# Kernel tuning notes

Measured on AMD Instinct MI355X. Metric: run time of the kernel, lower is better.

Reference implementation:

```python
import jax, jax.numpy as jnp
import numpy as np

D = 32        # number of TT cores (d)
R = 16        # tt_rank
B = 262144    # batch size


def setup_inputs() -> dict:
    key = jax.random.key(0)
    k1, k2, k3, k4 = jax.random.split(key, 4)
    return {
        "X": jax.random.randint(k1, (B, D), 0, 2, dtype=jnp.int32),
        "core_first": jax.random.normal(k2, (1, R, 2), dtype=jnp.float32),
        "cores_mid": jax.random.normal(k3, (D - 2, R, R, 2), dtype=jnp.float32),
        "core_last": jax.random.normal(k4, (R, 1, 2), dtype=jnp.float32),
    }


def reference(X, core_first, cores_mid, core_last):
    # First core: cores[0][:, :, X[:,0]] -> [1, R, B] -> permute -> [B, 1, R].
    # We carry the squeezed [B, R] row vector instead of [B, 1, R].
    carry0 = jnp.take(core_first[0], X[:, 0], axis=-1).T  # [B, R]

    def step(carry, inp):
        core, idx = inp                       # core: [R, R, 2], idx: [B]
        c = jnp.take(core, idx, axis=2)       # gathered core: [R, R, B]
        new = jnp.einsum('br,rsb->bs', carry, c)  # batched (1xR)@(RxR)
        return new, None

    # Middle cores i = 1 .. D-2 (sequential chain, data-dependent).
    carry, _ = jax.lax.scan(step, carry0, (cores_mid, X[:, 1:D - 1].T))

    # Last core: cores[-1][:, :, X[:,-1]] -> [R, 1, B]; contract to scalar per batch.
    c_last = jnp.take(core_last[:, 0, :], X[:, -1], axis=-1)  # [R, B]
    out = jnp.einsum('br,rb->b', carry, c_last)               # [B]  (squeeze of [B,1,1])
    return out
```

## Files before the change

kernel.cpp:

```cpp
#include <hip/hip_runtime.h>


#define R 16
#define TT_D 32
#define BATCH 262144

#define OFF_V16  0
#define OFF_W16  1048576
#define OFF_P8   2097152
#define OFF_Q8   (OFF_P8 + 65536)
#define OFF_V8   (OFF_Q8 + 65536)
#define OFF_W8   (OFF_V8 + 4096)
#define OFF_PK   (OFF_W8 + 4096)
#define WS_FLOATS (OFF_PK + BATCH)

#define NBLK1 1024
#define NTAB  34

__device__ __forceinline__ void rowvec_mat(const float* __restrict__ M,
                                           float* __restrict__ u) {
    float nv[R];
    #pragma unroll
    for (int s = 0; s < R; s++) nv[s] = 0.f;
    #pragma unroll
    for (int t2 = 0; t2 < R; t2++) {
        const float a = u[t2];
        #pragma unroll
        for (int s = 0; s < R; s++) nv[s] += a * M[t2 * 16 + s];
    }
    #pragma unroll
    for (int s = 0; s < R; s++) u[s] = nv[s];
}

__device__ __forceinline__ void mat_colvec(const float* __restrict__ M,
                                           float* __restrict__ w) {
    float nw[R];
    #pragma unroll
    for (int r2 = 0; r2 < R; r2++) {
        float a = 0.f;
        #pragma unroll
        for (int k = 0; k < R; k++) a += M[r2 * 16 + k] * w[k];
        nw[r2] = a;
    }
    #pragma unroll
    for (int r2 = 0; r2 < R; r2++) w[r2] = nw[r2];
}

__global__ __launch_bounds__(256) void tt_stage1(const int* __restrict__ X,
                                                 const float* __restrict__ cf,
                                                 const float* __restrict__ cm,
                                                 const float* __restrict__ cl,
                                                 float* __restrict__ ws) {
    __shared__ float scm[8 * 512];
    const int blk = blockIdx.x;
    const int t = threadIdx.x;

    if (blk < NTAB) {
        int cbase, ncore;
        if (blk < 16)       { cbase = 7;  ncore = 8; }
        else if (blk < 32)  { cbase = 15; ncore = 8; }
        else if (blk == 32) { cbase = 0;  ncore = 7; }
        else                { cbase = 23; ncore = 7; }
        const float2* cm2 = (const float2*)(cm + cbase * 512);
        for (int j = t; j < ncore * 256; j += 256) {
            const float2 vv = cm2[j];
            const int ci = j >> 8, idx = j & 255;
            scm[ci * 512 + idx] = vv.x;
            scm[ci * 512 + 256 + idx] = vv.y;
        }
        __syncthreads();

        if (blk < 32) {
            const bool isP = (blk < 16);
            const int e = (isP ? blk : blk - 16) * 16 + (t >> 4), r = t & 15;
            float u[R];
            const float* M0 = scm + ((e >> 7) & 1) * 256;
            #pragma unroll
            for (int s = 0; s < R; s++) u[s] = M0[r * 16 + s];
            for (int k = 1; k < 8; k++)
                rowvec_mat(scm + k * 512 + ((e >> (7 - k)) & 1) * 256, u);
            float* o = ws + (isP ? OFF_P8 : OFF_Q8) + e * 256 + r * 16;
            #pragma unroll
            for (int s = 0; s < R; s++) o[s] = u[s];
        } else if (blk == 32) {
            const int e = t;
            float u[R];
            #pragma unroll
            for (int s = 0; s < R; s++) u[s] = cf[s * 2 + ((e >> 7) & 1)];
            for (int k = 0; k < 7; k++)
                rowvec_mat(scm + k * 512 + ((e >> (6 - k)) & 1) * 256, u);
            float* o = ws + OFF_V8 + e * 16;
            #pragma unroll
            for (int s = 0; s < R; s++) o[s] = u[s];
        } else {
            const int e = t;
            float w[R];
            #pragma unroll
            for (int r2 = 0; r2 < R; r2++) w[r2] = cl[r2 * 2 + (e & 1)];
            for (int j = 6; j >= 0; j--)
                mat_colvec(scm + j * 512 + ((e >> (7 - j)) & 1) * 256, w);
            float* o = ws + OFF_W8 + e * 16;
            #pragma unroll
            for (int r2 = 0; r2 < R; r2++) o[r2] = w[r2];
        }
    } else {
        unsigned* pk = (unsigned*)(ws + OFF_PK);
        const int stride = (NBLK1 - NTAB) * 256;
        for (int b = (blk - NTAB) * 256 + t; b < BATCH; b += stride) {
            const int4* Xr = (const int4*)(X + (size_t)b * TT_D);
            unsigned p = 0, s = 0;
            #pragma unroll
            for (int q = 0; q < 4; q++) {
                const int4 c = Xr[q];
                p = (p << 4) | ((unsigned)(c.x & 1) << 3) | ((unsigned)(c.y & 1) << 2)
                             | ((unsigned)(c.z & 1) << 1) | (unsigned)(c.w & 1);
            }
            #pragma unroll
            for (int q = 4; q < 8; q++) {
                const int4 c = Xr[q];
                s = (s << 4) | ((unsigned)(c.x & 1) << 3) | ((unsigned)(c.y & 1) << 2)
                             | ((unsigned)(c.z & 1) << 1) | (unsigned)(c.w & 1);
            }
            pk[b] = (p << 16) | s;
        }
    }
}

__global__ __launch_bounds__(256) void tt_stage2(float* __restrict__ ws) {
    __shared__ float sQ[256];
    const int blk = blockIdx.x;
    const int t = threadIdx.x;
    if (blk < 256) {
        const int hi = blk, lo = t;
        float u[R];
        const float* v8 = ws + OFF_V8 + hi * 16;
        #pragma unroll
        for (int k = 0; k < R; k++) u[k] = v8[k];
        rowvec_mat(ws + OFF_P8 + lo * 256, u);
        float* o = ws + OFF_V16 + (size_t)(hi * 256 + lo) * 16;
        #pragma unroll
        for (int s = 0; s < R; s++) o[s] = u[s];
    } else {
        const int hi = blk - 256, lo = t;
        sQ[t] = ws[OFF_Q8 + hi * 256 + t];
        __syncthreads();
        float w[R];
        const float* w8 = ws + OFF_W8 + lo * 16;
        #pragma unroll
        for (int k = 0; k < R; k++) w[k] = w8[k];
        mat_colvec(sQ, w);
        float* o = ws + OFF_W16 + (size_t)(hi * 256 + lo) * 16;
        #pragma unroll
        for (int r2 = 0; r2 < R; r2++) o[r2] = w[r2];
    }
}

__global__ __launch_bounds__(256) void tt_gather(const float* __restrict__ ws,
                                                 float* __restrict__ out) {
    const int b = blockIdx.x * 256 + threadIdx.x;
    const unsigned pk = ((const unsigned*)(ws + OFF_PK))[b];
    const unsigned p = pk >> 16, s = pk & 0xffffu;
    const float4* v = (const float4*)(ws + OFF_V16 + (size_t)p * 16);
    const float4* w = (const float4*)(ws + OFF_W16 + (size_t)s * 16);
    float acc = 0.f;
    #pragma unroll
    for (int k = 0; k < 4; k++) {
        const float4 a = v[k], c = w[k];
        acc += a.x * c.x + a.y * c.y + a.z * c.z + a.w * c.w;
    }
    out[b] = acc;
}

__global__ __launch_bounds__(256) void tt_direct(const int* __restrict__ X,
                                                 const float* __restrict__ cf,
                                                 const float* __restrict__ cm,
                                                 const float* __restrict__ cl,
                                                 float* __restrict__ out) {
    __shared__ float scm[30 * 16 * 16 * 2];
    for (int i = threadIdx.x; i < 30 * 16 * 16 * 2; i += blockDim.x) scm[i] = cm[i];
    __syncthreads();
    const int b = blockIdx.x * blockDim.x + threadIdx.x;
    if (b >= BATCH) return;
    const int* xr = X + (size_t)b * TT_D;
    float v[R], nv[R];
    const int x0 = xr[0] & 1;
    #pragma unroll
    for (int rr = 0; rr < R; rr++) v[rr] = cf[rr * 2 + x0];
    for (int i = 1; i <= 30; i++) {
        const int bit = xr[i] & 1;
        const float* M = scm + (i - 1) * 512;
        #pragma unroll
        for (int s2 = 0; s2 < R; s2++) {
            float acc = 0.f;
            #pragma unroll
            for (int rr = 0; rr < R; rr++) acc += v[rr] * M[(rr * 16 + s2) * 2 + bit];
            nv[s2] = acc;
        }
        #pragma unroll
        for (int s2 = 0; s2 < R; s2++) v[s2] = nv[s2];
    }
    const int xl = xr[31] & 1;
    float acc = 0.f;
    #pragma unroll
    for (int rr = 0; rr < R; rr++) acc += v[rr] * cl[rr * 2 + xl];
    out[b] = acc;
}

extern "C" void kernel_launch(void* const* d_in, const int* in_sizes, int n_in,
                              void* d_out, int out_size, void* d_ws, size_t ws_size,
                              hipStream_t stream) {
    const int* X = (const int*)d_in[0];
    const float* cf = (const float*)d_in[1];
    const float* cm = (const float*)d_in[2];
    const float* cl = (const float*)d_in[3];
    float* out = (float*)d_out;

    if (ws_size >= (size_t)WS_FLOATS * sizeof(float)) {
        float* ws = (float*)d_ws;
        tt_stage1<<<NBLK1, 256, 0, stream>>>(X, cf, cm, cl, ws);
        tt_stage2<<<512, 256, 0, stream>>>(ws);
        tt_gather<<<BATCH / 256, 256, 0, stream>>>(ws, out);
    } else {
        tt_direct<<<(BATCH + 255) / 256, 256, 0, stream>>>(X, cf, cm, cl, out);
    }
}
```

Baseline: 117.4 us.

## Fuse three stages into one cooperative kernel with grid syncs

Replaces the three launches (table build with X packing, table expansion, gather) with one cooperative kernel of 512 blocks that uses grid.sync between phases. Each thread packs its two batch elements' bits into registers before the first sync, so the packed-index array no longer goes through global memory. This is meant to remove launch gaps and the pack-array round trip. In exchange it adds two grid-wide barriers, and only 34 blocks do the table work in phase one. The old three-kernel path stays as a fallback if the cooperative launch fails.

Result: slower. 346.0 us (+194.7%).

```diff
diff --git a/kernel.cpp b/kernel.cpp
--- a/kernel.cpp
+++ b/kernel.cpp
@@ -1,21 +1,22 @@
 #include <hip/hip_runtime.h>
+#include <hip/hip_cooperative_groups.h>
+
+namespace cg = cooperative_groups;
 
 
 #define R 16
 #define TT_D 32
 #define BATCH 262144
-
-#define OFF_V16  0
-#define OFF_W16  1048576
-#define OFF_P8   2097152
-#define OFF_Q8   (OFF_P8 + 65536)
+#define NBLK 512
+#define EPB (BATCH / NBLK)
+
+#define OFF_P8   0
+#define OFF_Q8   65536
 #define OFF_V8   (OFF_Q8 + 65536)
 #define OFF_W8   (OFF_V8 + 4096)
-#define OFF_PK   (OFF_W8 + 4096)
-#define WS_FLOATS (OFF_PK + BATCH)
-
-#define NBLK1 1024
-#define NTAB  34
+#define OFF_V16  (OFF_W8 + 4096)
+#define OFF_W16  (OFF_V16 + 1048576)
+#define WS_FLOATS (OFF_W16 + 1048576)
 
 __device__ __forceinline__ void rowvec_mat(const float* __restrict__ M,
                                            float* __restrict__ u) {
@@ -46,16 +47,33 @@
     for (int r2 = 0; r2 < R; r2++) w[r2] = nw[r2];
 }
 
-__global__ __launch_bounds__(256) void tt_stage1(const int* __restrict__ X,
-                                                 const float* __restrict__ cf,
-                                                 const float* __restrict__ cm,
-                                                 const float* __restrict__ cl,
-                                                 float* __restrict__ ws) {
+__device__ __forceinline__ unsigned pack_elem(const int* __restrict__ X, int b) {
+    const int4* Xr = (const int4*)(X + (size_t)b * TT_D);
+    unsigned v = 0;
+    #pragma unroll
+    for (int q = 0; q < 8; q++) {
+        const int4 c = Xr[q];
+        v = (v << 4) | ((unsigned)(c.x & 1) << 3) | ((unsigned)(c.y & 1) << 2)
+                     | ((unsigned)(c.z & 1) << 1) | (unsigned)(c.w & 1);
+    }
+    return v;
+}
+
+__global__ __launch_bounds__(256, 2) void tt_fused(const int* __restrict__ X,
+                                                   const float* __restrict__ cf,
+                                                   const float* __restrict__ cm,
+                                                   const float* __restrict__ cl,
+                                                   float* __restrict__ ws,
+                                                   float* __restrict__ out) {
     __shared__ float scm[8 * 512];
     const int blk = blockIdx.x;
     const int t = threadIdx.x;
-
-    if (blk < NTAB) {
+    cg::grid_group grid = cg::this_grid();
+
+    const unsigned pk0 = pack_elem(X, blk * EPB + t);
+    const unsigned pk1 = pack_elem(X, blk * EPB + 256 + t);
+
+    if (blk < 34) {
         int cbase, ncore;
         if (blk < 16)       { cbase = 7;  ncore = 8; }
         else if (blk < 32)  { cbase = 15; ncore = 8; }
@@ -103,26 +121,122 @@
             #pragma unroll
             for (int r2 = 0; r2 < R; r2++) o[r2] = w[r2];
         }
+    }
+
+    __threadfence();
+    grid.sync();
+
+    if (blk < 256) {
+        float u[R];
+        const float* v8 = ws + OFF_V8 + blk * 16;
+        #pragma unroll
+        for (int k = 0; k < R; k++) u[k] = v8[k];
+        rowvec_mat(ws + OFF_P8 + t * 256, u);
+        float* o = ws + OFF_V16 + (size_t)(blk * 256 + t) * 16;
+        #pragma unroll
+        for (int s = 0; s < R; s++) o[s] = u[s];
     } else {
-        unsigned* pk = (unsigned*)(ws + OFF_PK);
-        const int stride = (NBLK1 - NTAB) * 256;
-        for (int b = (blk - NTAB) * 256 + t; b < BATCH; b += stride) {
-            const int4* Xr = (const int4*)(X + (size_t)b * TT_D);
-            unsigned p = 0, s = 0;
-            #pragma unroll
-            for (int q = 0; q < 4; q++) {
-                const int4 c = Xr[q];
-                p = (p << 4) | ((unsigned)(c.x & 1) << 3) | ((unsigned)(c.y & 1) << 2)
-                             | ((unsigned)(c.z & 1) << 1) | (unsigned)(c.w & 1);
-            }
-            #pragma unroll
-            for (int q = 4; q < 8; q++) {
-                const int4 c = Xr[q];
-                s = (s << 4) | ((unsigned)(c.x & 1) << 3) | ((unsigned)(c.y & 1) << 2)
-                             | ((unsigned)(c.z & 1) << 1) | (unsigned)(c.w & 1);
-            }
-            pk[b] = (p << 16) | s;
-        }
+        const int hi = blk - 256;
+        __syncthreads();
+        scm[t] = ws[OFF_Q8 + hi * 256 + t];
+        __syncthreads();
+        float w[R];
+        const float* w8 = ws + OFF_W8 + t * 16;
+        #pragma unroll
+        for (int k = 0; k < R; k++) w[k] = w8[k];
+        mat_colvec(scm, w);
+        float* o = ws + OFF_W16 + (size_t)(hi * 256 + t) * 16;
+        #pragma unroll
+        for (int r2 = 0; r2 < R; r2++) o[r2] = w[r2];
+    }
+
+    __threadfence();
+    grid.sync();
+
+    {
+        const float4* v = (const float4*)(ws + OFF_V16 + (size_t)(pk0 >> 16) * 16);
+        const float4* w = (const float4*)(ws + OFF_W16 + (size_t)(pk0 & 0xffffu) * 16);
+        float acc = 0.f;
+        #pragma unroll
+        for (int k = 0; k < 4; k++) {
+            const float4 a = v[k], c = w[k];
+            acc += a.x * c.x + a.y * c.y + a.z * c.z + a.w * c.w;
+        }
+        out[blk * EPB + t] = acc;
+    }
+    {
+        const float4* v = (const float4*)(ws + OFF_V16 + (size_t)(pk1 >> 16) * 16);
+        const float4* w = (const float4*)(ws + OFF_W16 + (size_t)(pk1 & 0xffffu) * 16);
+        float acc = 0.f;
+        #pragma unroll
+        for (int k = 0; k < 4; k++) {
+            const float4 a = v[k], c = w[k];
+            acc += a.x * c.x + a.y * c.y + a.z * c.z + a.w * c.w;
+        }
+        out[blk * EPB + 256 + t] = acc;
+    }
+}
+
+__global__ __launch_bounds__(256) void tt_stage1(const int* __restrict__ X,
+                                                 const float* __restrict__ cf,
+                                                 const float* __restrict__ cm,
+                                                 const float* __restrict__ cl,
+                                                 float* __restrict__ ws,
+                                                 unsigned* __restrict__ pk) {
+    __shared__ float scm[8 * 512];
+    const int blk = blockIdx.x;
+    const int t = threadIdx.x;
+    if (blk < 34) {
+        int cbase, ncore;
+        if (blk < 16)       { cbase = 7;  ncore = 8; }
+        else if (blk < 32)  { cbase = 15; ncore = 8; }
+        else if (blk == 32) { cbase = 0;  ncore = 7; }
+        else                { cbase = 23; ncore = 7; }
+        const float2* cm2 = (const float2*)(cm + cbase * 512);
+        for (int j = t; j < ncore * 256; j += 256) {
+            const float2 vv = cm2[j];
+            const int ci = j >> 8, idx = j & 255;
+            scm[ci * 512 + idx] = vv.x;
+            scm[ci * 512 + 256 + idx] = vv.y;
+        }
+        __syncthreads();
+        if (blk < 32) {
+            const bool isP = (blk < 16);
+            const int e = (isP ? blk : blk - 16) * 16 + (t >> 4), r = t & 15;
+            float u[R];
+            const float* M0 = scm + ((e >> 7) & 1) * 256;
+            #pragma unroll
+            for (int s = 0; s < R; s++) u[s] = M0[r * 16 + s];
+            for (int k = 1; k < 8; k++)
+                rowvec_mat(scm + k * 512 + ((e >> (7 - k)) & 1) * 256, u);
+            float* o = ws + (isP ? OFF_P8 : OFF_Q8) + e * 256 + r * 16;
+            #pragma unroll
+            for (int s = 0; s < R; s++) o[s] = u[s];
+        } else if (blk == 32) {
+            const int e = t;
+            float u[R];
+            #pragma unroll
+            for (int s = 0; s < R; s++) u[s] = cf[s * 2 + ((e >> 7) & 1)];
+            for (int k = 0; k < 7; k++)
+                rowvec_mat(scm + k * 512 + ((e >> (6 - k)) & 1) * 256, u);
+            float* o = ws + OFF_V8 + e * 16;
+            #pragma unroll
+            for (int s = 0; s < R; s++) o[s] = u[s];
+        } else {
+            const int e = t;
+            float w[R];
+            #pragma unroll
+            for (int r2 = 0; r2 < R; r2++) w[r2] = cl[r2 * 2 + (e & 1)];
+            for (int j = 6; j >= 0; j--)
+                mat_colvec(scm + j * 512 + ((e >> (7 - j)) & 1) * 256, w);
+            float* o = ws + OFF_W8 + e * 16;
+            #pragma unroll
+            for (int r2 = 0; r2 < R; r2++) o[r2] = w[r2];
+        }
+    } else {
+        const int stride = (1024 - 34) * 256;
+        for (int b = (blk - 34) * 256 + t; b < BATCH; b += stride)
+            pk[b] = pack_elem(X, b);
     }
 }
 
@@ -131,37 +245,36 @@
     const int blk = blockIdx.x;
     const int t = threadIdx.x;
     if (blk < 256) {
-        const int hi = blk, lo = t;
         float u[R];
-        const float* v8 = ws + OFF_V8 + hi * 16;
+        const float* v8 = ws + OFF_V8 + blk * 16;
         #pragma unroll
         for (int k = 0; k < R; k++) u[k] = v8[k];
-        rowvec_mat(ws + OFF_P8 + lo * 256, u);
-        float* o = ws + OFF_V16 + (size_t)(hi * 256 + lo) * 16;
+        rowvec_mat(ws + OFF_P8 + t * 256, u);
+        float* o = ws + OFF_V16 + (size_t)(blk * 256 + t) * 16;
         #pragma unroll
         for (int s = 0; s < R; s++) o[s] = u[s];
     } else {
-        const int hi = blk - 256, lo = t;
+        const int hi = blk - 256;
         sQ[t] = ws[OFF_Q8 + hi * 256 + t];
         __syncthreads();
         float w[R];
-        const float* w8 = ws + OFF_W8 + lo * 16;
+        const float* w8 = ws + OFF_W8 + t * 16;
         #pragma unroll
         for (int k = 0; k < R; k++) w[k] = w8[k];
         mat_colvec(sQ, w);
-        float* o = ws + OFF_W16 + (size_t)(hi * 256 + lo) * 16;
+        float* o = ws + OFF_W16 + (size_t)(hi * 256 + t) * 16;
         #pragma unroll
         for (int r2 = 0; r2 < R; r2++) o[r2] = w[r2];
     }
 }
 
 __global__ __launch_bounds__(256) void tt_gather(const float* __restrict__ ws,
+                                                 const unsigned* __restrict__ pk,
                                                  float* __restrict__ out) {
     const int b = blockIdx.x * 256 + threadIdx.x;
-    const unsigned pk = ((const unsigned*)(ws + OFF_PK))[b];
-    const unsigned p = pk >> 16, s = pk & 0xffffu;
-    const float4* v = (const float4*)(ws + OFF_V16 + (size_t)p * 16);
-    const float4* w = (const float4*)(ws + OFF_W16 + (size_t)s * 16);
+    const unsigned v2 = pk[b];
+    const float4* v = (const float4*)(ws + OFF_V16 + (size_t)(v2 >> 16) * 16);
+    const float4* w = (const float4*)(ws + OFF_W16 + (size_t)(v2 & 0xffffu) * 16);
     float acc = 0.f;
     #pragma unroll
     for (int k = 0; k < 4; k++) {
@@ -215,11 +328,20 @@
     const float* cl = (const float*)d_in[3];
     float* out = (float*)d_out;
 
-    if (ws_size >= (size_t)WS_FLOATS * sizeof(float)) {
+    const size_t need = ((size_t)WS_FLOATS + BATCH) * sizeof(float);
+    if (ws_size >= need) {
         float* ws = (float*)d_ws;
-        tt_stage1<<<NBLK1, 256, 0, stream>>>(X, cf, cm, cl, ws);
-        tt_stage2<<<512, 256, 0, stream>>>(ws);
-        tt_gather<<<BATCH / 256, 256, 0, stream>>>(ws, out);
+        void* args[] = { (void*)&X, (void*)&cf, (void*)&cm, (void*)&cl,
+                         (void*)&ws, (void*)&out };
+        hipError_t err = hipLaunchCooperativeKernel((const void*)tt_fused,
+                                                    dim3(NBLK), dim3(256),
+                                                    args, 0, stream);
+        if (err != hipSuccess) {
+            unsigned* pk = (unsigned*)(ws + WS_FLOATS);
+            tt_stage1<<<1024, 256, 0, stream>>>(X, cf, cm, cl, ws, pk);
+            tt_stage2<<<512, 256, 0, stream>>>(ws);
+            tt_gather<<<BATCH / 256, 256, 0, stream>>>(ws, pk, out);
+        }
     } else {
         tt_direct<<<(BATCH + 255) / 256, 256, 0, stream>>>(X, cf, cm, cl, out);
     }
```
